# Kernel optimization log

Measured on AMD Instinct MI355X. Metric: run time of the kernel, lower is better.

## Reference

```python
import jax, jax.numpy as jnp
import numpy as np

DIM = 768
HEADS = 12
HEAD_DIM = DIM // HEADS
SCALE = HEAD_DIM ** -0.5
ALPHA = 0.1


def setup_inputs() -> dict:
    key = jax.random.key(0)
    ks = jax.random.split(key, 6)
    B, N, C = 16, 577, DIM
    x = jax.random.normal(ks[0], (B, N, C), dtype=jnp.float32)
    attn_weight = jax.random.uniform(ks[1], (B, N - 1), dtype=jnp.float32)
    w_qkv = jax.random.normal(ks[2], (C, 3 * C), dtype=jnp.float32) * (C ** -0.5)
    b_qkv = jnp.zeros((3 * C,), dtype=jnp.float32)
    w_proj = jax.random.normal(ks[3], (C, C), dtype=jnp.float32) * (C ** -0.5)
    b_proj = jnp.zeros((C,), dtype=jnp.float32)
    return {"x": x, "attn_weight": attn_weight, "w_qkv": w_qkv, "b_qkv": b_qkv,
            "w_proj": w_proj, "b_proj": b_proj}


def reference(x, attn_weight, w_qkv, b_qkv, w_proj, b_proj):
    B, N, C = x.shape
    H, D = HEADS, HEAD_DIM
    qkv = (x @ w_qkv + b_qkv).reshape(B, N, 3, H, D)
    qkv = jnp.transpose(qkv, (2, 0, 3, 1, 4))  # [3, B, H, N, D]
    q, k, v = qkv[0], qkv[1], qkv[2]
    attn = jnp.einsum('bhnd,bhmd->bhnm', q, k) * SCALE  # [B,H,N,N]
    patch_attn = attn[:, :, 0, 1:]  # pre-softmax CLS->patch scores
    # reweight CLS row (excluding CLS->CLS) before softmax
    w = attn_weight[:, None, None, :]  # [B,1,1,N-1]
    cls_row = attn[:, :, 0:1, 1:] * (w * ALPHA + (1.0 - ALPHA))
    attn = attn.at[:, :, 0:1, 1:].set(cls_row)
    attn = jax.nn.softmax(attn, axis=-1)
    out = jnp.einsum('bhnm,bhmd->bhnd', attn, v)
    out = jnp.transpose(out, (0, 2, 1, 3)).reshape(B, N, C)
    out = out @ w_proj + b_proj
    return out, patch_attn
```

## Files before the change

kernel.cpp:

```cpp
#include <hip/hip_runtime.h>
#include <hip/hip_bf16.h>
#include <math.h>

#define B_    16
#define N_    577
#define C_    768
#define H_    12
#define D_    64
#define M_    (B_ * N_)
#define MP_   9344
#define QKVN  2304
#define NP_   640
#define SCALE 0.125f
#define ALPHA 0.1f
#define OUT0  (B_ * N_ * C_)

#define NB_CONV 7008
#define NB_T1   1728
#define NB_T2   576

typedef __attribute__((ext_vector_type(8))) short short8;
typedef __attribute__((ext_vector_type(4))) float f32x4;
typedef __hip_bfloat16 bf16;

__device__ __forceinline__ float exp2fast(float x) {
    return __builtin_amdgcn_exp2f(x);
}

__device__ __forceinline__ void load16(const void* g, void* l) {
    __builtin_amdgcn_global_load_lds(
        (const __attribute__((address_space(1))) unsigned int*)g,
        (__attribute__((address_space(3))) unsigned int*)l, 16, 0, 0);
}

__device__ __forceinline__ f32x4 mfma16(short8 a, short8 b, f32x4 c) {
    return __builtin_amdgcn_mfma_f32_16x16x32_bf16(a, b, c, 0, 0, 0);
}

__global__ __launch_bounds__(256) void prep(const float* __restrict__ x,
                                            bf16* __restrict__ xb,
                                            const float* __restrict__ wq,
                                            bf16* __restrict__ wqT,
                                            const float* __restrict__ wp,
                                            bf16* __restrict__ wpT) {
    __shared__ float tile[32][33];
    const int bid = blockIdx.x;
    if (bid < NB_CONV) {
        int idx = bid * 256 + threadIdx.x;
        int m = idx / 192;
        bf16 tmp[4];
        if (m < M_) {
            float4 f = ((const float4*)x)[idx];
            tmp[0] = __float2bfloat16(f.x);
            tmp[1] = __float2bfloat16(f.y);
            tmp[2] = __float2bfloat16(f.z);
            tmp[3] = __float2bfloat16(f.w);
        } else {
            tmp[0] = tmp[1] = tmp[2] = tmp[3] = __float2bfloat16(0.f);
        }
        ((ushort4*)xb)[idx] = *(ushort4*)tmp;
        return;
    }
    const float* src; bf16* dst; int C, R, bx, by;
    if (bid < NB_CONV + NB_T1) {
        int r = bid - NB_CONV;
        bx = r % 72; by = r / 72; src = wq; dst = wqT; R = 768; C = QKVN;
    } else {
        int r = bid - NB_CONV - NB_T1;
        bx = r % 24; by = r / 24; src = wp; dst = wpT; R = 768; C = 768;
    }
    int cb = bx * 32, rb = by * 32;
    int tx = threadIdx.x & 31, ty = threadIdx.x >> 5;
    #pragma unroll
    for (int i = 0; i < 32; i += 8)
        tile[ty + i][tx] = src[(size_t)(rb + ty + i) * C + cb + tx];
    __syncthreads();
    #pragma unroll
    for (int i = 0; i < 32; i += 8)
        dst[(size_t)(cb + ty + i) * R + rb + tx] = __float2bfloat16(tile[tx][ty + i]);
}

__global__ __launch_bounds__(256) void gemm_bt(const bf16* __restrict__ A,
                                               const bf16* __restrict__ BT,
                                               const float* __restrict__ bias,
                                               bf16* __restrict__ q,
                                               bf16* __restrict__ kk,
                                               bf16* __restrict__ vt,
                                               float* __restrict__ out,
                                               int mode, int nby) {
    __shared__ __align__(16) char smem[35840];
    bf16* Tt = (bf16*)smem;

    const int L = blockIdx.x;
    const int xcd = L & 7;
    const int li = L >> 3;
    const int mi = li % 10;
    const int nb = li / 10;
    const int slab = (xcd == 0) ? 10 : 9;
    if (mi >= slab) return;
    const int mb = (xcd == 0) ? mi : (10 + (xcd - 1) * 9 + mi);

    const int m0 = mb * 128, n0 = nb * 128;
    const int t = threadIdx.x, lane = t & 63, w = t >> 6;
    const int wr = w >> 1, wc = w & 1;
    const int rsel = lane & 15, ksel = (lane >> 4) * 8;
    const int r16 = lane & 15, quad = lane >> 4;

    f32x4 acc[4][4];
    #pragma unroll
    for (int i = 0; i < 4; i++)
        #pragma unroll
        for (int j = 0; j < 4; j++) acc[i][j] = (f32x4)(0.f);

    const int srow = w * 32 + (lane >> 2);
    const int scol = (lane & 3) * 8;
    const bf16* ga = A  + (size_t)(m0 + srow) * 768 + scol;
    const bf16* gb = BT + (size_t)(n0 + srow) * 768 + scol;
    const int loff = w * 1024 + lane * 8;

    uint4 ra0, ra1, rb0, rb1;
    auto fetch = [&](int kt) {
        int gc = kt * 32;
        ra0 = *(const uint4*)(ga + gc);
        ra1 = *(const uint4*)(ga + gc + 16 * 768);
        rb0 = *(const uint4*)(gb + gc);
        rb1 = *(const uint4*)(gb + gc + 16 * 768);
    };
    auto commit = [&](int buf) {
        bf16* dstA = (bf16*)(smem + buf * 16384);
        bf16* dstB = dstA + 4096;
        *(uint4*)(dstA + loff)       = ra0;
        *(uint4*)(dstA + loff + 512) = ra1;
        *(uint4*)(dstB + loff)       = rb0;
        *(uint4*)(dstB + loff + 512) = rb1;
    };

    fetch(0);
    commit(0);
    __syncthreads();

    for (int kt = 0; kt < 24; kt++) {
        const int cur = kt & 1;
        if (kt < 23) fetch(kt + 1);

        const bf16* As = (const bf16*)(smem + cur * 16384);
        const bf16* Bs = As + 4096;
        short8 af[4], bfg[4];
        #pragma unroll
        for (int mi2 = 0; mi2 < 4; mi2++)
            af[mi2] = *(const short8*)(As + (wr * 64 + mi2 * 16 + rsel) * 32 + ksel);
        #pragma unroll
        for (int nj = 0; nj < 4; nj++)
            bfg[nj] = *(const short8*)(Bs + (wc * 64 + nj * 16 + rsel) * 32 + ksel);
        #pragma unroll
        for (int mi2 = 0; mi2 < 4; mi2++)
            #pragma unroll
            for (int nj = 0; nj < 4; nj++)
                acc[mi2][nj] = mfma16(af[mi2], bfg[nj], acc[mi2][nj]);

        if (kt < 23) commit(cur ^ 1);
        __syncthreads();
    }

    float bs[4];
    #pragma unroll
    for (int nj = 0; nj < 4; nj++) bs[nj] = bias[n0 + wc * 64 + nj * 16 + r16];

    if (mode == 1) {
        const int row0 = quad * 4;
        #pragma unroll
        for (int mi2 = 0; mi2 < 4; mi2++) {
            #pragma unroll
            for (int nj = 0; nj < 4; nj++) {
                #pragma unroll
                for (int r = 0; r < 4; r++) {
                    int m = m0 + wr * 64 + mi2 * 16 + row0 + r;
                    if (m >= M_) continue;
                    int cc = n0 + wc * 64 + nj * 16 + r16;
                    out[(size_t)m * 768 + cc] = acc[mi2][nj][r] + bs[nj];
                }
            }
        }
        return;
    }

    #pragma unroll
    for (int mi2 = 0; mi2 < 4; mi2++) {
        #pragma unroll
        for (int nj = 0; nj < 4; nj++) {
            bf16 pk[4];
            #pragma unroll
            for (int r = 0; r < 4; r++)
                pk[r] = __float2bfloat16(acc[mi2][nj][r] + bs[nj]);
            int ccl = wc * 64 + nj * 16 + r16;
            int ml4 = wr * 64 + mi2 * 16 + quad * 4;
            *(uint2*)&Tt[ccl * 140 + ml4] = *(const uint2*)pk;
        }
    }
    __syncthreads();

    const int part = nb / 6;
    if (part < 2) {
        int nl = t & 127, half = t >> 7;
        int m = m0 + nl;
        if (m < M_) {
            int b = m / N_, n = m - b * N_;
            int h = (nb % 6) * 2 + half;
            bf16* dst = (part == 0 ? q : kk) + ((size_t)(b * H_ + h) * N_ + n) * 64;
            #pragma unroll
            for (int d8 = 0; d8 < 8; d8++) {
                bf16 tv[8];
                #pragma unroll
                for (int dd = 0; dd < 8; dd++)
                    tv[dd] = Tt[(half * 64 + d8 * 8 + dd) * 140 + nl];
                *(uint4*)(dst + d8 * 8) = *(const uint4*)tv;
            }
        }
    } else {
        int dr = t >> 1, seg = t & 1;
        int rem = (nb % 6) * 128 + dr;
        int h = rem >> 6, d = rem & 63;
        int mb2 = m0 + seg * 64;
        int b = mb2 / N_;
        int n = mb2 - b * N_;
        const bf16* src = Tt + dr * 140 + seg * 64;
        int i = 0;
        while (i < 64 && mb2 + i < M_) {
            if (n == N_) { b++; n = 0; }
            bf16* drow = vt + ((size_t)(b * H_ + h) * 64 + d) * NP_;
            if ((n & 7) == 0 && n + 8 <= N_ && i + 8 <= 64 && mb2 + i + 8 <= M_) {
                bf16 tv[8];
                #pragma unroll
                for (int dd = 0; dd < 8; dd++) tv[dd] = src[i + dd];
                *(uint4*)(drow + n) = *(const uint4*)tv;
                i += 8; n += 8;
            } else {
                drow[n] = src[i]; i++; n++;
            }
        }
    }
}

__global__ __launch_bounds__(256) void attn_mfma(const bf16* __restrict__ q,
                                                 const bf16* __restrict__ k,
                                                 const bf16* __restrict__ vt,
                                                 const float* __restrict__ aw,
                                                 bf16* __restrict__ ao,
                                                 float* __restrict__ patch) {
    __shared__ bf16 Kb[2][4096];
    __shared__ bf16 Vb[2][4096];
    __shared__ bf16 Pb[4][2048];
    const int bh = blockIdx.x, qt = blockIdx.y;
    const int b = bh / H_, h = bh - b * H_;
    const int t = threadIdx.x, lane = t & 63, w = t >> 6;
    const int r16 = lane & 15, quad = lane >> 4;
    const float SC2 = SCALE * 1.44269504f;

    const bf16* kbp = k + (size_t)bh * N_ * 64;
    const bf16* vbp = vt + (size_t)bh * 64 * NP_;

    short8 qa0[2], qa1[2];
    #pragma unroll
    for (int mi = 0; mi < 2; mi++) {
        int qrow = qt * 128 + w * 32 + mi * 16 + r16;
        int qrc = (qrow < N_) ? qrow : (N_ - 1);
        const bf16* qp = q + ((size_t)bh * N_ + qrc) * 64 + quad * 8;
        qa0[mi] = *(const short8*)(qp);
        qa1[mi] = *(const short8*)(qp + 32);
    }

    f32x4 Oacc[2][4];
    #pragma unroll
    for (int mi = 0; mi < 2; mi++)
        #pragma unroll
        for (int d0 = 0; d0 < 4; d0++) Oacc[mi][d0] = (f32x4)(0.f);
    float lrow[2][4];
    #pragma unroll
    for (int mi = 0; mi < 2; mi++)
        #pragma unroll
        for (int rr = 0; rr < 4; rr++) lrow[mi][rr] = 0.f;

    const bool clsrow = (qt == 0) && (w == 0) && (quad == 0);

    auto stage = [&](int kt, int buf) {
        #pragma unroll
        for (int is = 0; is < 2; is++) {
            int base = is * 256 + w * 64;
            int slot = base + lane;
            int row = slot >> 3, pos = slot & 7;
            int c = pos ^ (row & 7);
            int jg = kt * 64 + row; if (jg > N_ - 1) jg = N_ - 1;
            load16(kbp + (size_t)jg * 64 + c * 8, &Kb[buf][base * 8]);
        }
        #pragma unroll
        for (int is = 0; is < 2; is++) {
            int base = is * 256 + w * 64;
            int slot = base + lane;
            int row = slot >> 3, pos = slot & 7;
            int c = pos ^ (row & 7);
            load16(vbp + (size_t)row * NP_ + kt * 64 + c * 8, &Vb[buf][base * 8]);
        }
    };

    stage(0, 0);
    __syncthreads();

    for (int kt = 0; kt < 10; kt++) {
        const int cur = kt & 1;
        if (kt < 9) stage(kt + 1, cur ^ 1);

        f32x4 S[2][4];
        #pragma unroll
        for (int j0 = 0; j0 < 4; j0++) {
            int row = j0 * 16 + r16;
            const bf16* kpl = &Kb[cur][row * 64];
            short8 kf0 = *(const short8*)(kpl + ((quad ^ (row & 7)) << 3));
            short8 kf1 = *(const short8*)(kpl + (((quad ^ 4) ^ (row & 7)) << 3));
            #pragma unroll
            for (int mi = 0; mi < 2; mi++) {
                f32x4 sa = (f32x4)(0.f);
                sa = mfma16(qa0[mi], kf0, sa);
                sa = mfma16(qa1[mi], kf1, sa);
                S[mi][j0] = sa;
            }
        }

        if (kt < 9) {
            #pragma unroll
            for (int mi = 0; mi < 2; mi++) {
                #pragma unroll
                for (int j0 = 0; j0 < 4; j0++) {
                    float wfac = 1.f;
                    if (mi == 0 && clsrow) {
                        int c = kt * 64 + j0 * 16 + r16;
                        if (c >= 1) {
                            patch[(size_t)bh * (N_ - 1) + (c - 1)] = S[0][j0][0] * SCALE;
                            wfac = aw[b * (N_ - 1) + (c - 1)] * ALPHA + (1.f - ALPHA);
                        }
                    }
                    #pragma unroll
                    for (int rr = 0; rr < 4; rr++) {
                        float v = S[mi][j0][rr] * SC2;
                        if (rr == 0) v *= wfac;
                        float p = exp2fast(v);
                        S[mi][j0][rr] = p;
                        lrow[mi][rr] += p;
                    }
                }
            }
        } else {
            #pragma unroll
            for (int mi = 0; mi < 2; mi++) {
                #pragma unroll
                for (int j0 = 0; j0 < 4; j0++) {
                    int c = kt * 64 + j0 * 16 + r16;
                    bool valid = (c < N_);
                    float wfac = 1.f;
                    if (mi == 0 && clsrow && valid) {
                        patch[(size_t)bh * (N_ - 1) + (c - 1)] = S[0][j0][0] * SCALE;
                        wfac = aw[b * (N_ - 1) + (c - 1)] * ALPHA + (1.f - ALPHA);
                    }
                    #pragma unroll
                    for (int rr = 0; rr < 4; rr++) {
                        float v = S[mi][j0][rr] * SC2;
                        if (rr == 0) v *= wfac;
                        float p = valid ? exp2fast(v) : 0.f;
                        S[mi][j0][rr] = p;
                        lrow[mi][rr] += p;
                    }
                }
            }
        }

        bf16* pw = &Pb[w][0];
        #pragma unroll
        for (int mi = 0; mi < 2; mi++) {
            #pragma unroll
            for (int j0 = 0; j0 < 4; j0++) {
                int cg = j0 * 2 + (r16 >> 3);
                #pragma unroll
                for (int rr = 0; rr < 4; rr++) {
                    int rp = mi * 16 + quad * 4 + rr;
                    pw[rp * 64 + ((cg ^ (rp & 7)) << 3) + (r16 & 7)] =
                        __float2bfloat16(S[mi][j0][rr]);
                }
            }
        }
        short8 pa0[2], pa1[2];
        #pragma unroll
        for (int mi = 0; mi < 2; mi++) {
            int rp = mi * 16 + r16;
            const bf16* pr = pw + rp * 64;
            pa0[mi] = *(const short8*)(pr + ((quad ^ (rp & 7)) << 3));
            pa1[mi] = *(const short8*)(pr + (((quad ^ 4) ^ (rp & 7)) << 3));
        }

        #pragma unroll
        for (int d0 = 0; d0 < 4; d0++) {
            int row = d0 * 16 + r16;
            const bf16* vpl = &Vb[cur][row * 64];
            short8 vf0 = *(const short8*)(vpl + ((quad ^ (row & 7)) << 3));
            short8 vf1 = *(const short8*)(vpl + (((quad ^ 4) ^ (row & 7)) << 3));
            #pragma unroll
            for (int mi = 0; mi < 2; mi++) {
                Oacc[mi][d0] = mfma16(pa0[mi], vf0, Oacc[mi][d0]);
                Oacc[mi][d0] = mfma16(pa1[mi], vf1, Oacc[mi][d0]);
            }
        }
        __syncthreads();
    }

    #pragma unroll
    for (int mi = 0; mi < 2; mi++) {
        #pragma unroll
        for (int rr = 0; rr < 4; rr++) {
            float l = lrow[mi][rr];
            l += __shfl_xor(l, 1);
            l += __shfl_xor(l, 2);
            l += __shfl_xor(l, 4);
            l += __shfl_xor(l, 8);
            int n = qt * 128 + w * 32 + mi * 16 + quad * 4 + rr;
            if (n >= N_) continue;
            float inv = 1.f / l;
            #pragma unroll
            for (int d0 = 0; d0 < 4; d0++) {
                ao[((size_t)(b * N_ + n) * H_ + h) * 64 + d0 * 16 + r16] =
                    __float2bfloat16(Oacc[mi][d0][rr] * inv);
            }
        }
    }
}

extern "C" void kernel_launch(void* const* d_in, const int* in_sizes, int n_in,
                              void* d_out, int out_size, void* d_ws, size_t ws_size,
                              hipStream_t stream) {
    const float* x      = (const float*)d_in[0];
    const float* aw     = (const float*)d_in[1];
    const float* w_qkv  = (const float*)d_in[2];
    const float* b_qkv  = (const float*)d_in[3];
    const float* w_proj = (const float*)d_in[4];
    const float* b_proj = (const float*)d_in[5];
    float* out = (float*)d_out;

    char* ws = (char*)d_ws;
    bf16* xbf    = (bf16*)(ws);
    bf16* wqkvT  = (bf16*)(ws + 14352384);
    bf16* wprojT = (bf16*)(ws + 17891328);
    bf16* qv     = (bf16*)(ws + 19070976);
    bf16* kv     = (bf16*)(ws + 33251328);
    bf16* vt     = (bf16*)(ws + 47431680);
    bf16* ao     = xbf;

    prep<<<NB_CONV + NB_T1 + NB_T2, 256, 0, stream>>>(x, xbf, w_qkv, wqkvT, w_proj, wprojT);

    gemm_bt<<<8 * 10 * 18, 256, 0, stream>>>(
        xbf, wqkvT, b_qkv, qv, kv, vt, nullptr, 0, 18);

    attn_mfma<<<dim3(H_ * B_, 5), 256, 0, stream>>>(qv, kv, vt, aw, ao, out + OUT0);

    gemm_bt<<<8 * 10 * 6, 256, 0, stream>>>(
        ao, wprojT, b_proj, nullptr, nullptr, nullptr, out, 1, 6);
}
```

Measured before the change: 221.2 us.

## Replace 128x128 GEMM with 256x256 tile kernel using direct-to-LDS loads

Replaces the 128x128-tile, 256-thread GEMM with a 256x256-tile, 512-thread kernel used for both the QKV and output projections. Tiles are staged with global_load_lds into a swizzled LDS layout with 64-wide K steps, double buffered. The main loop is split into four phases separated by explicit barriers and raised wave priority around the MFMA blocks. The goal is more data reuse per loaded byte and less LDS bank conflict and VGPR staging overhead. In exchange it drops the XCD-aware block mapping and launches far fewer blocks (111 for the output projection), which can leave compute units idle. The last M tile also reads A rows past the padded buffer.

```diff
diff --git a/kernel.cpp b/kernel.cpp
--- a/kernel.cpp
+++ b/kernel.cpp
@@ -36,6 +36,10 @@
 __device__ __forceinline__ f32x4 mfma16(short8 a, short8 b, f32x4 c) {
     return __builtin_amdgcn_mfma_f32_16x16x32_bf16(a, b, c, 0, 0, 0);
 }
+
+#define FENCE() asm volatile("" ::: "memory")
+#define BARRIER() do { FENCE(); __builtin_amdgcn_s_barrier(); FENCE(); } while (0)
+#define WAITLGKM0() asm volatile("s_waitcnt lgkmcnt(0)" ::: "memory")
 
 __global__ __launch_bounds__(256) void prep(const float* __restrict__ x,
                                             bf16* __restrict__ xb,
@@ -80,86 +84,123 @@
         dst[(size_t)(cb + ty + i) * R + rb + tx] = __float2bfloat16(tile[tx][ty + i]);
 }
 
-__global__ __launch_bounds__(256) void gemm_bt(const bf16* __restrict__ A,
-                                               const bf16* __restrict__ BT,
-                                               const float* __restrict__ bias,
-                                               bf16* __restrict__ q,
-                                               bf16* __restrict__ kk,
-                                               bf16* __restrict__ vt,
-                                               float* __restrict__ out,
-                                               int mode, int nby) {
-    __shared__ __align__(16) char smem[35840];
-    bf16* Tt = (bf16*)smem;
-
-    const int L = blockIdx.x;
-    const int xcd = L & 7;
-    const int li = L >> 3;
-    const int mi = li % 10;
-    const int nb = li / 10;
-    const int slab = (xcd == 0) ? 10 : 9;
-    if (mi >= slab) return;
-    const int mb = (xcd == 0) ? mi : (10 + (xcd - 1) * 9 + mi);
-
-    const int m0 = mb * 128, n0 = nb * 128;
+__global__ __launch_bounds__(512, 2) void gemm256(const bf16* __restrict__ A,
+                                                  const bf16* __restrict__ BT,
+                                                  const float* __restrict__ bias,
+                                                  bf16* __restrict__ q,
+                                                  bf16* __restrict__ kk,
+                                                  bf16* __restrict__ vt,
+                                                  float* __restrict__ out,
+                                                  int mode, int nby) {
+    __shared__ __align__(16) char smem[131072];
+
+    const int bid = blockIdx.x;
+    const int mb = bid / nby;
+    const int nb = bid % nby;
+    const int m0 = mb * 256, n0 = nb * 256;
     const int t = threadIdx.x, lane = t & 63, w = t >> 6;
-    const int wr = w >> 1, wc = w & 1;
-    const int rsel = lane & 15, ksel = (lane >> 4) * 8;
+    const int wr = w >> 2, wc = w & 3;
     const int r16 = lane & 15, quad = lane >> 4;
 
-    f32x4 acc[4][4];
-    #pragma unroll
-    for (int i = 0; i < 4; i++)
+    f32x4 acc[8][4];
+    #pragma unroll
+    for (int i = 0; i < 8; i++)
         #pragma unroll
         for (int j = 0; j < 4; j++) acc[i][j] = (f32x4)(0.f);
 
-    const int srow = w * 32 + (lane >> 2);
-    const int scol = (lane & 3) * 8;
-    const bf16* ga = A  + (size_t)(m0 + srow) * 768 + scol;
-    const bf16* gb = BT + (size_t)(n0 + srow) * 768 + scol;
-    const int loff = w * 1024 + lane * 8;
-
-    uint4 ra0, ra1, rb0, rb1;
-    auto fetch = [&](int kt) {
-        int gc = kt * 32;
-        ra0 = *(const uint4*)(ga + gc);
-        ra1 = *(const uint4*)(ga + gc + 16 * 768);
-        rb0 = *(const uint4*)(gb + gc);
-        rb1 = *(const uint4*)(gb + gc + 16 * 768);
+    const int lrow = lane >> 3;
+    const int clog = ((lane & 7) ^ lrow) << 4;
+    const int s2 = w * 2;
+    const char* gA = (const char*)A  + (size_t)(m0 + lrow) * 1536 + clog;
+    const char* gB = (const char*)BT + (size_t)(n0 + lrow) * 1536 + clog;
+
+    auto stA = [&](int kt2, int half) {
+        int ro = (half * 128 + s2 * 8) * 1536 + kt2 * 128;
+        char* d = (char*)smem + (kt2 & 1) * 32768 + half * 16384 + s2 * 1024;
+        load16(gA + ro, d);
+        load16(gA + ro + 8 * 1536, d + 1024);
     };
-    auto commit = [&](int buf) {
-        bf16* dstA = (bf16*)(smem + buf * 16384);
-        bf16* dstB = dstA + 4096;
-        *(uint4*)(dstA + loff)       = ra0;
-        *(uint4*)(dstA + loff + 512) = ra1;
-        *(uint4*)(dstB + loff)       = rb0;
-        *(uint4*)(dstB + loff + 512) = rb1;
+    auto stB = [&](int kt2, int half) {
+        int ro = (half * 128 + s2 * 8) * 1536 + kt2 * 128;
+        char* d = (char*)smem + 65536 + (kt2 & 1) * 32768 + half * 16384 + s2 * 1024;
+        load16(gB + ro, d);
+        load16(gB + ro + 8 * 1536, d + 1024);
     };
 
-    fetch(0);
-    commit(0);
-    __syncthreads();
-
-    for (int kt = 0; kt < 24; kt++) {
+    stA(0, 0); stA(0, 1); stB(0, 0); stB(0, 1);
+    stA(1, 0); stA(1, 1);
+    asm volatile("s_waitcnt vmcnt(4)" ::: "memory");
+    BARRIER();
+
+    const int sw = r16 & 7;
+    const int g0 = (quad ^ sw) << 4;
+    const int g1 = ((quad ^ 4) ^ sw) << 4;
+
+    short8 af0[8], af1[8], bq0[2], bq1[2];
+
+    #pragma unroll
+    for (int kt = 0; kt < 12; kt++) {
         const int cur = kt & 1;
-        if (kt < 23) fetch(kt + 1);
-
-        const bf16* As = (const bf16*)(smem + cur * 16384);
-        const bf16* Bs = As + 4096;
-        short8 af[4], bfg[4];
-        #pragma unroll
-        for (int mi2 = 0; mi2 < 4; mi2++)
-            af[mi2] = *(const short8*)(As + (wr * 64 + mi2 * 16 + rsel) * 32 + ksel);
-        #pragma unroll
-        for (int nj = 0; nj < 4; nj++)
-            bfg[nj] = *(const short8*)(Bs + (wc * 64 + nj * 16 + rsel) * 32 + ksel);
-        #pragma unroll
-        for (int mi2 = 0; mi2 < 4; mi2++)
-            #pragma unroll
-            for (int nj = 0; nj < 4; nj++)
-                acc[mi2][nj] = mfma16(af[mi2], bfg[nj], acc[mi2][nj]);
-
-        if (kt < 23) commit(cur ^ 1);
-        __syncthreads();
+        const char* Ap = (const char*)smem + cur * 32768 + (wr * 128 + r16) * 128;
+        const char* Bp = (const char*)smem + 65536 + cur * 32768 + (wc * 64 + r16) * 128;
+
+        #pragma unroll
+        for (int mi = 0; mi < 8; mi++) af0[mi] = *(const short8*)(Ap + mi * 2048 + g0);
+        bq0[0] = *(const short8*)(Bp + 0 * 2048 + g0);
+        bq0[1] = *(const short8*)(Bp + 1 * 2048 + g0);
+        if (kt < 11) stB(kt + 1, 0);
+        BARRIER();
+        WAITLGKM0();
+        __builtin_amdgcn_s_setprio(1);
+        #pragma unroll
+        for (int mi = 0; mi < 8; mi++) acc[mi][0] = mfma16(af0[mi], bq0[0], acc[mi][0]);
+        #pragma unroll
+        for (int mi = 0; mi < 8; mi++) acc[mi][1] = mfma16(af0[mi], bq0[1], acc[mi][1]);
+        __builtin_amdgcn_s_setprio(0);
+        BARRIER();
+
+        #pragma unroll
+        for (int mi = 0; mi < 8; mi++) af1[mi] = *(const short8*)(Ap + mi * 2048 + g1);
+        bq1[0] = *(const short8*)(Bp + 2 * 2048 + g0);
+        bq1[1] = *(const short8*)(Bp + 3 * 2048 + g0);
+        if (kt < 11) stB(kt + 1, 1);
+        BARRIER();
+        WAITLGKM0();
+        __builtin_amdgcn_s_setprio(1);
+        #pragma unroll
+        for (int mi = 0; mi < 8; mi++) acc[mi][2] = mfma16(af0[mi], bq1[0], acc[mi][2]);
+        #pragma unroll
+        for (int mi = 0; mi < 8; mi++) acc[mi][3] = mfma16(af0[mi], bq1[1], acc[mi][3]);
+        __builtin_amdgcn_s_setprio(0);
+        BARRIER();
+
+        bq0[0] = *(const short8*)(Bp + 0 * 2048 + g1);
+        bq0[1] = *(const short8*)(Bp + 1 * 2048 + g1);
+        if (kt < 10) stA(kt + 2, 0);
+        BARRIER();
+        WAITLGKM0();
+        __builtin_amdgcn_s_setprio(1);
+        #pragma unroll
+        for (int mi = 0; mi < 8; mi++) acc[mi][0] = mfma16(af1[mi], bq0[0], acc[mi][0]);
+        #pragma unroll
+        for (int mi = 0; mi < 8; mi++) acc[mi][1] = mfma16(af1[mi], bq0[1], acc[mi][1]);
+        __builtin_amdgcn_s_setprio(0);
+        BARRIER();
+
+        bq1[0] = *(const short8*)(Bp + 2 * 2048 + g1);
+        bq1[1] = *(const short8*)(Bp + 3 * 2048 + g1);
+        if (kt < 10) stA(kt + 2, 1);
+        BARRIER();
+        WAITLGKM0();
+        __builtin_amdgcn_s_setprio(1);
+        #pragma unroll
+        for (int mi = 0; mi < 8; mi++) acc[mi][2] = mfma16(af1[mi], bq1[0], acc[mi][2]);
+        #pragma unroll
+        for (int mi = 0; mi < 8; mi++) acc[mi][3] = mfma16(af1[mi], bq1[1], acc[mi][3]);
+        __builtin_amdgcn_s_setprio(0);
+        if (kt < 10) { asm volatile("s_waitcnt vmcnt(4)" ::: "memory"); }
+        else         { asm volatile("s_waitcnt vmcnt(0)" ::: "memory"); }
+        BARRIER();
     }
 
     float bs[4];
@@ -167,75 +208,80 @@
     for (int nj = 0; nj < 4; nj++) bs[nj] = bias[n0 + wc * 64 + nj * 16 + r16];
 
     if (mode == 1) {
-        const int row0 = quad * 4;
-        #pragma unroll
-        for (int mi2 = 0; mi2 < 4; mi2++) {
+        #pragma unroll
+        for (int mi = 0; mi < 8; mi++) {
             #pragma unroll
             for (int nj = 0; nj < 4; nj++) {
                 #pragma unroll
                 for (int r = 0; r < 4; r++) {
-                    int m = m0 + wr * 64 + mi2 * 16 + row0 + r;
+                    int m = m0 + wr * 128 + mi * 16 + quad * 4 + r;
                     if (m >= M_) continue;
-                    int cc = n0 + wc * 64 + nj * 16 + r16;
-                    out[(size_t)m * 768 + cc] = acc[mi2][nj][r] + bs[nj];
+                    out[(size_t)m * 768 + n0 + wc * 64 + nj * 16 + r16] = acc[mi][nj][r] + bs[nj];
                 }
             }
         }
         return;
     }
 
-    #pragma unroll
-    for (int mi2 = 0; mi2 < 4; mi2++) {
-        #pragma unroll
-        for (int nj = 0; nj < 4; nj++) {
-            bf16 pk[4];
-            #pragma unroll
-            for (int r = 0; r < 4; r++)
-                pk[r] = __float2bfloat16(acc[mi2][nj][r] + bs[nj]);
-            int ccl = wc * 64 + nj * 16 + r16;
-            int ml4 = wr * 64 + mi2 * 16 + quad * 4;
-            *(uint2*)&Tt[ccl * 140 + ml4] = *(const uint2*)pk;
-        }
-    }
-    __syncthreads();
-
-    const int part = nb / 6;
-    if (part < 2) {
-        int nl = t & 127, half = t >> 7;
-        int m = m0 + nl;
-        if (m < M_) {
-            int b = m / N_, n = m - b * N_;
-            int h = (nb % 6) * 2 + half;
-            bf16* dst = (part == 0 ? q : kk) + ((size_t)(b * H_ + h) * N_ + n) * 64;
-            #pragma unroll
-            for (int d8 = 0; d8 < 8; d8++) {
-                bf16 tv[8];
+    bf16* Tt = (bf16*)smem;
+    const int part = nb / 3;
+    const int h0 = (nb % 3) * 4;
+
+    #pragma unroll
+    for (int rh = 0; rh < 2; rh++) {
+        __syncthreads();
+        if (wr == rh) {
+            #pragma unroll
+            for (int mi = 0; mi < 8; mi++) {
                 #pragma unroll
-                for (int dd = 0; dd < 8; dd++)
-                    tv[dd] = Tt[(half * 64 + d8 * 8 + dd) * 140 + nl];
-                *(uint4*)(dst + d8 * 8) = *(const uint4*)tv;
-            }
-        }
-    } else {
-        int dr = t >> 1, seg = t & 1;
-        int rem = (nb % 6) * 128 + dr;
-        int h = rem >> 6, d = rem & 63;
-        int mb2 = m0 + seg * 64;
-        int b = mb2 / N_;
-        int n = mb2 - b * N_;
-        const bf16* src = Tt + dr * 140 + seg * 64;
-        int i = 0;
-        while (i < 64 && mb2 + i < M_) {
-            if (n == N_) { b++; n = 0; }
-            bf16* drow = vt + ((size_t)(b * H_ + h) * 64 + d) * NP_;
-            if ((n & 7) == 0 && n + 8 <= N_ && i + 8 <= 64 && mb2 + i + 8 <= M_) {
-                bf16 tv[8];
+                for (int nj = 0; nj < 4; nj++) {
+                    bf16 pk[4];
+                    #pragma unroll
+                    for (int r = 0; r < 4; r++)
+                        pk[r] = __float2bfloat16(acc[mi][nj][r] + bs[nj]);
+                    int ccl = wc * 64 + nj * 16 + r16;
+                    int ml4 = mi * 16 + quad * 4;
+                    *(uint2*)&Tt[ccl * 140 + ml4] = *(const uint2*)pk;
+                }
+            }
+        }
+        __syncthreads();
+        if (part < 2) {
+            int nl = t & 127, hq = t >> 7;
+            int m = m0 + rh * 128 + nl;
+            if (m < M_) {
+                int b = m / N_, n = m - b * N_;
+                bf16* dst = (part == 0 ? q : kk) + ((size_t)(b * H_ + h0 + hq) * N_ + n) * 64;
                 #pragma unroll
-                for (int dd = 0; dd < 8; dd++) tv[dd] = src[i + dd];
-                *(uint4*)(drow + n) = *(const uint4*)tv;
-                i += 8; n += 8;
-            } else {
-                drow[n] = src[i]; i++; n++;
+                for (int d8 = 0; d8 < 8; d8++) {
+                    bf16 tv[8];
+                    #pragma unroll
+                    for (int dd = 0; dd < 8; dd++)
+                        tv[dd] = Tt[(hq * 64 + d8 * 8 + dd) * 140 + nl];
+                    *(uint4*)(dst + d8 * 8) = *(const uint4*)tv;
+                }
+            }
+        } else {
+            int dr = t >> 1, seg = t & 1;
+            int rem = (nb % 3) * 256 + dr;
+            int h = rem >> 6, d = rem & 63;
+            int mb2 = m0 + rh * 128 + seg * 64;
+            int b = mb2 / N_;
+            int n = mb2 - b * N_;
+            const bf16* src = Tt + dr * 140 + seg * 64;
+            int i = 0;
+            while (i < 64 && mb2 + i < M_) {
+                if (n == N_) { b++; n = 0; }
+                bf16* drow = vt + ((size_t)(b * H_ + h) * 64 + d) * NP_;
+                if ((n & 7) == 0 && n + 8 <= N_ && i + 8 <= 64 && mb2 + i + 8 <= M_) {
+                    bf16 tv[8];
+                    #pragma unroll
+                    for (int dd = 0; dd < 8; dd++) tv[dd] = src[i + dd];
+                    *(uint4*)(drow + n) = *(const uint4*)tv;
+                    i += 8; n += 8;
+                } else {
+                    drow[n] = src[i]; i++; n++;
+                }
             }
         }
     }
@@ -453,11 +499,11 @@
 
     prep<<<NB_CONV + NB_T1 + NB_T2, 256, 0, stream>>>(x, xbf, w_qkv, wqkvT, w_proj, wprojT);
 
-    gemm_bt<<<8 * 10 * 18, 256, 0, stream>>>(
-        xbf, wqkvT, b_qkv, qv, kv, vt, nullptr, 0, 18);
+    gemm256<<<37 * 9, 512, 0, stream>>>(
+        xbf, wqkvT, b_qkv, qv, kv, vt, nullptr, 0, 9);
 
     attn_mfma<<<dim3(H_ * B_, 5), 256, 0, stream>>>(qv, kv, vt, aw, ao, out + OUT0);
 
-    gemm_bt<<<8 * 10 * 6, 256, 0, stream>>>(
-        ao, wprojT, b_proj, nullptr, nullptr, nullptr, out, 1, 6);
-}
+    gemm256<<<37 * 3, 512, 0, stream>>>(
+        ao, wprojT, b_proj, nullptr, nullptr, nullptr, out, 1, 3);
+}
```

Result: slower. 229.3 us (+3.6%).

## Rewrite GEMM mainloop with direct global-to-LDS loads, swizzled LDS, deeper K tiles

Applied to the files above, without the earlier changes.

The 128x128 bf16 GEMM used for the QKV and output projections now uses global_load_lds to copy tiles straight into LDS, with an XOR-swizzled layout to avoid bank conflicts. The K step grows from 32 to 64 elements per stage, so there are 12 iterations instead of 24 and half as many barriers. It also raises MFMA issue priority with s_setprio and replaces the 8-way XCD slab mapping with a general contiguous XCD remap over 73 exact M-blocks, which drops the blocks that used to exit early. LDS use rises to 64KB per block with a two-blocks-per-CU launch bound, which may limit occupancy.

```diff
diff --git a/kernel.cpp b/kernel.cpp
--- a/kernel.cpp
+++ b/kernel.cpp
@@ -36,6 +36,9 @@
 __device__ __forceinline__ f32x4 mfma16(short8 a, short8 b, f32x4 c) {
     return __builtin_amdgcn_mfma_f32_16x16x32_bf16(a, b, c, 0, 0, 0);
 }
+
+#define FENCE() asm volatile("" ::: "memory")
+#define BARRIER() do { FENCE(); __builtin_amdgcn_s_barrier(); FENCE(); } while (0)
 
 __global__ __launch_bounds__(256) void prep(const float* __restrict__ x,
                                             bf16* __restrict__ xb,
@@ -80,30 +83,26 @@
         dst[(size_t)(cb + ty + i) * R + rb + tx] = __float2bfloat16(tile[tx][ty + i]);
 }
 
-__global__ __launch_bounds__(256) void gemm_bt(const bf16* __restrict__ A,
-                                               const bf16* __restrict__ BT,
-                                               const float* __restrict__ bias,
-                                               bf16* __restrict__ q,
-                                               bf16* __restrict__ kk,
-                                               bf16* __restrict__ vt,
-                                               float* __restrict__ out,
-                                               int mode, int nby) {
-    __shared__ __align__(16) char smem[35840];
-    bf16* Tt = (bf16*)smem;
-
-    const int L = blockIdx.x;
-    const int xcd = L & 7;
-    const int li = L >> 3;
-    const int mi = li % 10;
-    const int nb = li / 10;
-    const int slab = (xcd == 0) ? 10 : 9;
-    if (mi >= slab) return;
-    const int mb = (xcd == 0) ? mi : (10 + (xcd - 1) * 9 + mi);
-
+__global__ __launch_bounds__(256, 2) void gemm128(const bf16* __restrict__ A,
+                                                  const bf16* __restrict__ BT,
+                                                  const float* __restrict__ bias,
+                                                  bf16* __restrict__ q,
+                                                  bf16* __restrict__ kk,
+                                                  bf16* __restrict__ vt,
+                                                  float* __restrict__ out,
+                                                  int mode, int nby) {
+    __shared__ __align__(16) char smem[65536];
+
+    const int nwg = gridDim.x;
+    const int orig = blockIdx.x;
+    const int xcd = orig & 7, ii = orig >> 3;
+    const int qq = nwg >> 3, rr = nwg & 7;
+    const int wg = (xcd < rr ? xcd * (qq + 1) : rr * (qq + 1) + (xcd - rr) * qq) + ii;
+    const int mb = wg / nby;
+    const int nb = wg - mb * nby;
     const int m0 = mb * 128, n0 = nb * 128;
     const int t = threadIdx.x, lane = t & 63, w = t >> 6;
     const int wr = w >> 1, wc = w & 1;
-    const int rsel = lane & 15, ksel = (lane >> 4) * 8;
     const int r16 = lane & 15, quad = lane >> 4;
 
     f32x4 acc[4][4];
@@ -112,54 +111,65 @@
         #pragma unroll
         for (int j = 0; j < 4; j++) acc[i][j] = (f32x4)(0.f);
 
-    const int srow = w * 32 + (lane >> 2);
-    const int scol = (lane & 3) * 8;
-    const bf16* ga = A  + (size_t)(m0 + srow) * 768 + scol;
-    const bf16* gb = BT + (size_t)(n0 + srow) * 768 + scol;
-    const int loff = w * 1024 + lane * 8;
-
-    uint4 ra0, ra1, rb0, rb1;
-    auto fetch = [&](int kt) {
-        int gc = kt * 32;
-        ra0 = *(const uint4*)(ga + gc);
-        ra1 = *(const uint4*)(ga + gc + 16 * 768);
-        rb0 = *(const uint4*)(gb + gc);
-        rb1 = *(const uint4*)(gb + gc + 16 * 768);
+    const int lrow = lane >> 3;
+    const int clog = ((lane & 7) ^ lrow) << 4;
+    const char* gA = (const char*)A  + (size_t)(m0 + w * 32 + lrow) * 1536 + clog;
+    const char* gB = (const char*)BT + (size_t)(n0 + w * 32 + lrow) * 1536 + clog;
+
+    auto stage = [&](int k2) {
+        const int bo = (k2 & 1) * 32768;
+        const int kc = k2 * 128;
+        #pragma unroll
+        for (int i = 0; i < 4; i++) {
+            char* dA = (char*)smem + bo + w * 4096 + i * 1024;
+            load16(gA + (size_t)i * 12288 + kc, dA);
+            load16(gB + (size_t)i * 12288 + kc, dA + 16384);
+        }
     };
-    auto commit = [&](int buf) {
-        bf16* dstA = (bf16*)(smem + buf * 16384);
-        bf16* dstB = dstA + 4096;
-        *(uint4*)(dstA + loff)       = ra0;
-        *(uint4*)(dstA + loff + 512) = ra1;
-        *(uint4*)(dstB + loff)       = rb0;
-        *(uint4*)(dstB + loff + 512) = rb1;
-    };
-
-    fetch(0);
-    commit(0);
-    __syncthreads();
-
-    for (int kt = 0; kt < 24; kt++) {
-        const int cur = kt & 1;
-        if (kt < 23) fetch(kt + 1);
-
-        const bf16* As = (const bf16*)(smem + cur * 16384);
-        const bf16* Bs = As + 4096;
-        short8 af[4], bfg[4];
-        #pragma unroll
-        for (int mi2 = 0; mi2 < 4; mi2++)
-            af[mi2] = *(const short8*)(As + (wr * 64 + mi2 * 16 + rsel) * 32 + ksel);
-        #pragma unroll
-        for (int nj = 0; nj < 4; nj++)
-            bfg[nj] = *(const short8*)(Bs + (wc * 64 + nj * 16 + rsel) * 32 + ksel);
-        #pragma unroll
-        for (int mi2 = 0; mi2 < 4; mi2++)
+
+    stage(0);
+    asm volatile("s_waitcnt vmcnt(0)" ::: "memory");
+    BARRIER();
+
+    const int sw = r16 & 7;
+    const int g0 = (quad ^ sw) << 4;
+    const int g1 = ((quad ^ 4) ^ sw) << 4;
+
+    #pragma unroll 1
+    for (int k = 0; k < 12; k++) {
+        const int cur = k & 1;
+        const char* Ap = (const char*)smem + cur * 32768 + (wr * 64 + r16) * 128;
+        const char* Bp = (const char*)smem + cur * 32768 + 16384 + (wc * 64 + r16) * 128;
+
+        if (k < 11) stage(k + 1);
+
+        short8 a[4], b[4];
+        #pragma unroll
+        for (int mi = 0; mi < 4; mi++) a[mi] = *(const short8*)(Ap + mi * 2048 + g0);
+        #pragma unroll
+        for (int nj = 0; nj < 4; nj++) b[nj] = *(const short8*)(Bp + nj * 2048 + g0);
+        __builtin_amdgcn_s_setprio(1);
+        #pragma unroll
+        for (int mi = 0; mi < 4; mi++)
             #pragma unroll
             for (int nj = 0; nj < 4; nj++)
-                acc[mi2][nj] = mfma16(af[mi2], bfg[nj], acc[mi2][nj]);
-
-        if (kt < 23) commit(cur ^ 1);
-        __syncthreads();
+                acc[mi][nj] = mfma16(a[mi], b[nj], acc[mi][nj]);
+        __builtin_amdgcn_s_setprio(0);
+
+        #pragma unroll
+        for (int mi = 0; mi < 4; mi++) a[mi] = *(const short8*)(Ap + mi * 2048 + g1);
+        #pragma unroll
+        for (int nj = 0; nj < 4; nj++) b[nj] = *(const short8*)(Bp + nj * 2048 + g1);
+        __builtin_amdgcn_s_setprio(1);
+        #pragma unroll
+        for (int mi = 0; mi < 4; mi++)
+            #pragma unroll
+            for (int nj = 0; nj < 4; nj++)
+                acc[mi][nj] = mfma16(a[mi], b[nj], acc[mi][nj]);
+        __builtin_amdgcn_s_setprio(0);
+
+        if (k < 11) { asm volatile("s_waitcnt vmcnt(0)" ::: "memory"); }
+        BARRIER();
     }
 
     float bs[4];
@@ -167,33 +177,33 @@
     for (int nj = 0; nj < 4; nj++) bs[nj] = bias[n0 + wc * 64 + nj * 16 + r16];
 
     if (mode == 1) {
-        const int row0 = quad * 4;
-        #pragma unroll
-        for (int mi2 = 0; mi2 < 4; mi2++) {
+        #pragma unroll
+        for (int mi = 0; mi < 4; mi++) {
             #pragma unroll
             for (int nj = 0; nj < 4; nj++) {
                 #pragma unroll
                 for (int r = 0; r < 4; r++) {
-                    int m = m0 + wr * 64 + mi2 * 16 + row0 + r;
+                    int m = m0 + wr * 64 + mi * 16 + quad * 4 + r;
                     if (m >= M_) continue;
                     int cc = n0 + wc * 64 + nj * 16 + r16;
-                    out[(size_t)m * 768 + cc] = acc[mi2][nj][r] + bs[nj];
+                    out[(size_t)m * 768 + cc] = acc[mi][nj][r] + bs[nj];
                 }
             }
         }
         return;
     }
 
-    #pragma unroll
-    for (int mi2 = 0; mi2 < 4; mi2++) {
+    bf16* Tt = (bf16*)smem;
+    #pragma unroll
+    for (int mi = 0; mi < 4; mi++) {
         #pragma unroll
         for (int nj = 0; nj < 4; nj++) {
             bf16 pk[4];
             #pragma unroll
             for (int r = 0; r < 4; r++)
-                pk[r] = __float2bfloat16(acc[mi2][nj][r] + bs[nj]);
+                pk[r] = __float2bfloat16(acc[mi][nj][r] + bs[nj]);
             int ccl = wc * 64 + nj * 16 + r16;
-            int ml4 = wr * 64 + mi2 * 16 + quad * 4;
+            int ml4 = wr * 64 + mi * 16 + quad * 4;
             *(uint2*)&Tt[ccl * 140 + ml4] = *(const uint2*)pk;
         }
     }
@@ -453,11 +463,11 @@
 
     prep<<<NB_CONV + NB_T1 + NB_T2, 256, 0, stream>>>(x, xbf, w_qkv, wqkvT, w_proj, wprojT);
 
-    gemm_bt<<<8 * 10 * 18, 256, 0, stream>>>(
+    gemm128<<<73 * 18, 256, 0, stream>>>(
         xbf, wqkvT, b_qkv, qv, kv, vt, nullptr, 0, 18);
 
     attn_mfma<<<dim3(H_ * B_, 5), 256, 0, stream>>>(qv, kv, vt, aw, ao, out + OUT0);
 
-    gemm_bt<<<8 * 10 * 6, 256, 0, stream>>>(
+    gemm128<<<73 * 6, 256, 0, stream>>>(
         ao, wprojT, b_proj, nullptr, nullptr, nullptr, out, 1, 6);
 }
```

New measurement: 216.0 us. 1.02x faster.
